# Optimization experiments

Hardware: AMD Instinct MI355X
Metric: run time of the kernel (lower is better)

## Reference

```python
import jax, jax.numpy as jnp
import numpy as np

HIDDEN_DIM = 128
NEIGHBOR_K = 2
N_ROWS = 1_000_000
BATCH = 262_144


def setup_inputs() -> dict:
    key = jax.random.key(0)
    k1, k2, k3, k4 = jax.random.split(key, 4)
    D = HIDDEN_DIM
    cat = D * (2 * NEIGHBOR_K + 1)  # 640
    x_rows = jax.random.normal(k1, (N_ROWS, D), dtype=jnp.float32)
    seed_indices = jax.random.randint(k2, (BATCH,), 0, N_ROWS)
    # torch.nn.Linear params: W [out, in], b [out]
    W1 = jax.random.normal(k3, (D, cat), dtype=jnp.float32) * (1.0 / np.sqrt(cat))
    b1 = jnp.zeros((D,), dtype=jnp.float32)
    W2 = jax.random.normal(k4, (D, D), dtype=jnp.float32) * (1.0 / np.sqrt(D))
    b2 = jnp.zeros((D,), dtype=jnp.float32)
    return {"x_rows": x_rows, "seed_indices": seed_indices,
            "W1": W1, "b1": b1, "W2": W2, "b2": b2}


def reference(x_rows, seed_indices, W1, b1, W2, b2):
    N, D = x_rows.shape
    B = seed_indices.shape[0]
    offsets = jnp.arange(-NEIGHBOR_K, NEIGHBOR_K + 1)  # [2k+1]
    idx = jnp.clip(seed_indices[:, None] + offsets[None, :], 0, N - 1)  # [B, 2k+1]
    # gather neighbor rows and flatten -> same as torch.cat(chunks, dim=-1)
    x_cat = x_rows[idx].reshape(B, (2 * NEIGHBOR_K + 1) * D)  # [B, 5D]
    h = jax.nn.relu(x_cat @ W1.T + b1)  # [B, D]
    return h @ W2.T + b2  # [B, D]
```

## Files before the change

kernel.cpp:

```cpp
#include <hip/hip_runtime.h>
#include <hip/hip_bf16.h>

#define D 128
#define CAT 640
#define BM 32
#define W1F_ELEMS 81920
#define W2F_ELEMS 16384

typedef __attribute__((ext_vector_type(8))) short bf16x8;
typedef __attribute__((ext_vector_type(4))) float f32x4;

static __device__ __forceinline__ unsigned short f32_to_bf16(float f) {
    unsigned u = __float_as_uint(f);
    unsigned r = u + 0x7FFFu + ((u >> 16) & 1u);
    return (unsigned short)(r >> 16);
}

static __device__ __forceinline__ unsigned pack_bf16x2(float a, float b) {
    __hip_bfloat162 h = __float22bfloat162_rn(make_float2(a, b));
    return *reinterpret_cast<unsigned*>(&h);
}

static __device__ __forceinline__ void gload_lds16(const float* g, void* lds) {
    __builtin_amdgcn_global_load_lds(
        (const __attribute__((address_space(1))) void*)g,
        (__attribute__((address_space(3))) void*)lds, 16, 0, 0);
}

__global__ void prep_frags(const float* __restrict__ W1, const float* __restrict__ W2,
                           unsigned short* __restrict__ W1f, unsigned short* __restrict__ W2f) {
    int f = blockIdx.x * 256 + threadIdx.x;
    if (f < W1F_ELEMS) {
        int e = f & 7, l = (f >> 3) & 63, j16 = (f >> 9) & 7, ks = f >> 12;
        int o = j16 * 16 + (l & 15);
        int k = ks * 32 + ((l >> 4) << 3) + e;
        W1f[f] = f32_to_bf16(W1[o * CAT + k]);
    } else if (f < W1F_ELEMS + W2F_ELEMS) {
        int f2 = f - W1F_ELEMS;
        int e = f2 & 7, l = (f2 >> 3) & 63, j16 = (f2 >> 9) & 7, ks = f2 >> 12;
        int o = j16 * 16 + (l & 15);
        int k = ks * 32 + ((l >> 4) << 3) + e;
        W2f[f2] = f32_to_bf16(W2[o * D + k]);
    }
}

__global__ __launch_bounds__(256, 4) void rowmlp_kernel(
    const float* __restrict__ x_rows, const int* __restrict__ seeds,
    const unsigned short* __restrict__ W1f, const float* __restrict__ b1,
    const unsigned short* __restrict__ W2f, const float* __restrict__ b2,
    float* __restrict__ out, int Nrows)
{
    __shared__ __align__(16) unsigned char Ab[2][16384];
    __shared__ int sseed[BM];

    const int tid = threadIdx.x;
    const int blk = blockIdx.x;
    const int w   = tid >> 6;
    const int l   = tid & 63;
    const int l15 = l & 15;
    const int lhi = l >> 4;

    if (tid < BM) sseed[tid] = seeds[blk * BM + tid];
    __syncthreads();

    const int sb  = sseed[((w >> 1) << 4) + l15];
    const int ksb = (w & 1) * 2;

    const bf16x8* W1v = (const bf16x8*)W1f;
    const bf16x8* W2v = (const bf16x8*)W2f;

#define WAIT0 asm volatile("s_waitcnt vmcnt(0)" ::: "memory")
#define BAR   __builtin_amdgcn_s_barrier()

#define ISSUE(J, BUF)                                                          \
    {                                                                          \
        int idx = sb + (J) - 2;                                                \
        idx = idx < 0 ? 0 : (idx >= Nrows ? Nrows - 1 : idx);                  \
        const float* rp = x_rows + (size_t)idx * D + lhi * 8;                  \
        unsigned char* dst = Ab[BUF] + w * 4096;                               \
        gload_lds16(rp + (ksb + 0) * 32 + 0, dst + 0 * 1024);                  \
        gload_lds16(rp + (ksb + 0) * 32 + 4, dst + 1 * 1024);                  \
        gload_lds16(rp + (ksb + 1) * 32 + 0, dst + 2 * 1024);                  \
        gload_lds16(rp + (ksb + 1) * 32 + 4, dst + 3 * 1024);                  \
    }

#define COMPUTE(BUF, J)                                                        \
    {                                                                          \
        const float* fb = (const float*)Ab[BUF];                               \
        _Pragma("unroll")                                                      \
        for (int ks = 0; ks < 4; ++ks) {                                       \
            bf16x8 a[2];                                                       \
            _Pragma("unroll")                                                  \
            for (int m = 0; m < 2; ++m) {                                      \
                float4 q0 = *(const float4*)(fb + (m * 8 + ks * 2 + 0) * 256 + l * 4); \
                float4 q1 = *(const float4*)(fb + (m * 8 + ks * 2 + 1) * 256 + l * 4); \
                union { unsigned u[4]; bf16x8 v; } pk;                         \
                pk.u[0] = pack_bf16x2(q0.x, q0.y);                             \
                pk.u[1] = pack_bf16x2(q0.z, q0.w);                             \
                pk.u[2] = pack_bf16x2(q1.x, q1.y);                             \
                pk.u[3] = pack_bf16x2(q1.z, q1.w);                             \
                a[m] = pk.v;                                                   \
            }                                                                  \
            _Pragma("unroll")                                                  \
            for (int n = 0; n < 2; ++n) {                                      \
                bf16x8 b = W1v[(((J) * 4 + ks) * 8 + (w * 2 + n)) * 64 + l];   \
                _Pragma("unroll")                                              \
                for (int m = 0; m < 2; ++m)                                    \
                    acc[m][n] = __builtin_amdgcn_mfma_f32_16x16x32_bf16(       \
                        a[m], b, acc[m][n], 0, 0, 0);                          \
            }                                                                  \
        }                                                                      \
    }

    f32x4 acc[2][2] = {};

    ISSUE(0, 0)

    WAIT0; BAR;
    ISSUE(1, 1)
    COMPUTE(0, 0)
    WAIT0; BAR;
    ISSUE(2, 0)
    COMPUTE(1, 1)
    WAIT0; BAR;
    ISSUE(3, 1)
    COMPUTE(0, 2)
    WAIT0; BAR;
    ISSUE(4, 0)
    COMPUTE(1, 3)
    WAIT0; BAR;
    COMPUTE(0, 4)

    unsigned short (*Hb)[D] = (unsigned short (*)[D])Ab[1];
    #pragma unroll
    for (int n = 0; n < 2; ++n) {
        const int col = w * 32 + n * 16 + l15;
        const float bias = b1[col];
        #pragma unroll
        for (int m = 0; m < 2; ++m) {
            #pragma unroll
            for (int r = 0; r < 4; ++r) {
                float v = acc[m][n][r] + bias;
                v = v > 0.f ? v : 0.f;
                const int row = m * 16 + lhi * 4 + r;
                Hb[row][col ^ ((row & 7) << 3)] = f32_to_bf16(v);
            }
        }
    }
    __syncthreads();

    f32x4 acc2[2][2] = {};
    #pragma unroll
    for (int ks = 0; ks < 4; ++ks) {
        bf16x8 a2[2], bb[2];
        #pragma unroll
        for (int m = 0; m < 2; ++m) {
            const int row = m * 16 + l15;
            a2[m] = *(const bf16x8*)(&Hb[row][(ks * 32 + lhi * 8) ^ ((row & 7) << 3)]);
        }
        #pragma unroll
        for (int n = 0; n < 2; ++n) {
            const int j16 = w * 2 + n;
            bb[n] = W2v[(ks * 8 + j16) * 64 + l];
        }
        #pragma unroll
        for (int m = 0; m < 2; ++m)
            #pragma unroll
            for (int n = 0; n < 2; ++n)
                acc2[m][n] = __builtin_amdgcn_mfma_f32_16x16x32_bf16(a2[m], bb[n], acc2[m][n], 0, 0, 0);
    }

    #pragma unroll
    for (int n = 0; n < 2; ++n) {
        const int col = w * 32 + n * 16 + l15;
        const float bias = b2[col];
        #pragma unroll
        for (int m = 0; m < 2; ++m) {
            #pragma unroll
            for (int r = 0; r < 4; ++r) {
                const int row = m * 16 + lhi * 4 + r;
                out[(size_t)(blk * BM + row) * D + col] = acc2[m][n][r] + bias;
            }
        }
    }
#undef ISSUE
#undef COMPUTE
#undef WAIT0
#undef BAR
}

extern "C" void kernel_launch(void* const* d_in, const int* in_sizes, int n_in,
                              void* d_out, int out_size, void* d_ws, size_t ws_size,
                              hipStream_t stream) {
    const float* x_rows = (const float*)d_in[0];
    const int*   seeds  = (const int*)d_in[1];
    const float* W1     = (const float*)d_in[2];
    const float* b1     = (const float*)d_in[3];
    const float* W2     = (const float*)d_in[4];
    const float* b2     = (const float*)d_in[5];
    float* out = (float*)d_out;

    int Nrows = in_sizes[0] / D;
    int B = in_sizes[1];

    unsigned short* W1f = (unsigned short*)d_ws;
    unsigned short* W2f = W1f + W1F_ELEMS;

    prep_frags<<<(W1F_ELEMS + W2F_ELEMS + 255) / 256, 256, 0, stream>>>(W1, W2, W1f, W2f);
    rowmlp_kernel<<<B / BM, 256, 0, stream>>>(x_rows, seeds, W1f, b1, W2f, b2, out, Nrows);
}
```

Measured before the change: 215.4 us.

## Coalesce row gathers with XOR-swizzled LDS layout and prefetch W1 fragments

Changes the gather so each half-wave loads one full contiguous 512-byte row of x_rows instead of scattered 32-byte pieces. The LDS copy uses an XOR swizzle so the MFMA A-operand reads stay free of bank conflicts. W1 fragments for the next neighbor slice are now loaded into a double-buffered register array while the current slice is computed, hiding their global latency. This raises register pressure (16 extra bf16x8 vectors), which may affect occupancy under launch_bounds(256,4); the second-layer accumulator reuses acc to offset part of that.

```diff
diff --git a/kernel.cpp b/kernel.cpp
--- a/kernel.cpp
+++ b/kernel.cpp
@@ -50,21 +50,27 @@
     const unsigned short* __restrict__ W2f, const float* __restrict__ b2,
     float* __restrict__ out, int Nrows)
 {
-    __shared__ __align__(16) unsigned char Ab[2][16384];
+    __shared__ __align__(16) unsigned char smem[2][16384];
     __shared__ int sseed[BM];
 
     const int tid = threadIdx.x;
     const int blk = blockIdx.x;
+
+    if (tid < BM) sseed[tid] = seeds[blk * BM + tid];
+    __syncthreads();
+
     const int w   = tid >> 6;
     const int l   = tid & 63;
     const int l15 = l & 15;
     const int lhi = l >> 4;
 
-    if (tid < BM) sseed[tid] = seeds[blk * BM + tid];
-    __syncthreads();
-
-    const int sb  = sseed[((w >> 1) << 4) + l15];
-    const int ksb = (w & 1) * 2;
+    int sbase[4], scoff[4];
+    #pragma unroll
+    for (int i = 0; i < 4; ++i) {
+        int r = 8 * w + 2 * i + (l >> 5);
+        sbase[i] = sseed[r];
+        scoff[i] = ((l & 31) ^ (r & 7)) << 2;
+    }
 
     const bf16x8* W1v = (const bf16x8*)W1f;
     const bf16x8* W2v = (const bf16x8*)W2f;
@@ -72,28 +78,39 @@
 #define WAIT0 asm volatile("s_waitcnt vmcnt(0)" ::: "memory")
 #define BAR   __builtin_amdgcn_s_barrier()
 
-#define ISSUE(J, BUF)                                                          \
+#define ISSUE(J)                                                               \
     {                                                                          \
-        int idx = sb + (J) - 2;                                                \
-        idx = idx < 0 ? 0 : (idx >= Nrows ? Nrows - 1 : idx);                  \
-        const float* rp = x_rows + (size_t)idx * D + lhi * 8;                  \
-        unsigned char* dst = Ab[BUF] + w * 4096;                               \
-        gload_lds16(rp + (ksb + 0) * 32 + 0, dst + 0 * 1024);                  \
-        gload_lds16(rp + (ksb + 0) * 32 + 4, dst + 1 * 1024);                  \
-        gload_lds16(rp + (ksb + 1) * 32 + 0, dst + 2 * 1024);                  \
-        gload_lds16(rp + (ksb + 1) * 32 + 4, dst + 3 * 1024);                  \
-    }
-
-#define COMPUTE(BUF, J)                                                        \
+        _Pragma("unroll")                                                      \
+        for (int i = 0; i < 4; ++i) {                                          \
+            int idx = sbase[i] + (J) - 2;                                      \
+            idx = idx < 0 ? 0 : (idx >= Nrows ? Nrows - 1 : idx);              \
+            gload_lds16(x_rows + (size_t)idx * D + scoff[i],                   \
+                        (void*)(smem[(J) & 1] + w * 4096 + i * 1024));         \
+        }                                                                      \
+    }
+
+#define LOADW1(J, RB)                                                          \
     {                                                                          \
-        const float* fb = (const float*)Ab[BUF];                               \
+        _Pragma("unroll")                                                      \
+        for (int ks = 0; ks < 4; ++ks)                                         \
+            _Pragma("unroll")                                                  \
+            for (int n = 0; n < 2; ++n)                                        \
+                w1r[RB][ks][n] = W1v[(((J) * 4 + ks) * 8 + (w * 2 + n)) * 64 + l]; \
+    }
+
+#define COMPUTE(BUF, RB)                                                       \
+    {                                                                          \
+        const float* buf = (const float*)smem[BUF];                            \
         _Pragma("unroll")                                                      \
         for (int ks = 0; ks < 4; ++ks) {                                       \
             bf16x8 a[2];                                                       \
             _Pragma("unroll")                                                  \
             for (int m = 0; m < 2; ++m) {                                      \
-                float4 q0 = *(const float4*)(fb + (m * 8 + ks * 2 + 0) * 256 + l * 4); \
-                float4 q1 = *(const float4*)(fb + (m * 8 + ks * 2 + 1) * 256 + l * 4); \
+                const int r = m * 16 + l15;                                    \
+                const int s = r & 7;                                           \
+                const int cc = ks * 8 + lhi * 2;                               \
+                float4 q0 = *(const float4*)(buf + r * 128 + (((cc) ^ s) << 2));     \
+                float4 q1 = *(const float4*)(buf + r * 128 + (((cc + 1) ^ s) << 2)); \
                 union { unsigned u[4]; bf16x8 v; } pk;                         \
                 pk.u[0] = pack_bf16x2(q0.x, q0.y);                             \
                 pk.u[1] = pack_bf16x2(q0.z, q0.w);                             \
@@ -102,36 +119,36 @@
                 a[m] = pk.v;                                                   \
             }                                                                  \
             _Pragma("unroll")                                                  \
-            for (int n = 0; n < 2; ++n) {                                      \
-                bf16x8 b = W1v[(((J) * 4 + ks) * 8 + (w * 2 + n)) * 64 + l];   \
+            for (int n = 0; n < 2; ++n)                                        \
                 _Pragma("unroll")                                              \
                 for (int m = 0; m < 2; ++m)                                    \
                     acc[m][n] = __builtin_amdgcn_mfma_f32_16x16x32_bf16(       \
-                        a[m], b, acc[m][n], 0, 0, 0);                          \
-            }                                                                  \
+                        a[m], w1r[RB][ks][n], acc[m][n], 0, 0, 0);             \
         }                                                                      \
     }
 
+    bf16x8 w1r[2][4][2];
     f32x4 acc[2][2] = {};
 
-    ISSUE(0, 0)
-
-    WAIT0; BAR;
-    ISSUE(1, 1)
+    ISSUE(0)
+    LOADW1(0, 0)
+
+    WAIT0; BAR;
+    ISSUE(1) LOADW1(1, 1)
     COMPUTE(0, 0)
     WAIT0; BAR;
-    ISSUE(2, 0)
+    ISSUE(2) LOADW1(2, 0)
     COMPUTE(1, 1)
     WAIT0; BAR;
-    ISSUE(3, 1)
-    COMPUTE(0, 2)
-    WAIT0; BAR;
-    ISSUE(4, 0)
-    COMPUTE(1, 3)
-    WAIT0; BAR;
-    COMPUTE(0, 4)
-
-    unsigned short (*Hb)[D] = (unsigned short (*)[D])Ab[1];
+    ISSUE(3) LOADW1(3, 1)
+    COMPUTE(0, 0)
+    WAIT0; BAR;
+    ISSUE(4) LOADW1(4, 0)
+    COMPUTE(1, 1)
+    WAIT0; BAR;
+    COMPUTE(0, 0)
+
+    unsigned short (*Hb)[D] = (unsigned short (*)[D])smem[1];
     #pragma unroll
     for (int n = 0; n < 2; ++n) {
         const int col = w * 32 + n * 16 + l15;
@@ -149,7 +166,11 @@
     }
     __syncthreads();
 
-    f32x4 acc2[2][2] = {};
+    #pragma unroll
+    for (int m = 0; m < 2; ++m)
+        #pragma unroll
+        for (int n = 0; n < 2; ++n)
+            acc[m][n] = (f32x4){0.f, 0.f, 0.f, 0.f};
     #pragma unroll
     for (int ks = 0; ks < 4; ++ks) {
         bf16x8 a2[2], bb[2];
@@ -167,7 +188,7 @@
         for (int m = 0; m < 2; ++m)
             #pragma unroll
             for (int n = 0; n < 2; ++n)
-                acc2[m][n] = __builtin_amdgcn_mfma_f32_16x16x32_bf16(a2[m], bb[n], acc2[m][n], 0, 0, 0);
+                acc[m][n] = __builtin_amdgcn_mfma_f32_16x16x32_bf16(a2[m], bb[n], acc[m][n], 0, 0, 0);
     }
 
     #pragma unroll
@@ -179,11 +200,12 @@
             #pragma unroll
             for (int r = 0; r < 4; ++r) {
                 const int row = m * 16 + lhi * 4 + r;
-                out[(size_t)(blk * BM + row) * D + col] = acc2[m][n][r] + bias;
+                out[(size_t)(blk * BM + row) * D + col] = acc[m][n][r] + bias;
             }
         }
     }
 #undef ISSUE
+#undef LOADW1
 #undef COMPUTE
 #undef WAIT0
 #undef BAR
```

After: 183.2 us, median of 2. 15.0% less time.
